# Optimization experiments

Measured on AMD Instinct MI355X. Metric: run time of the kernel, lower is better.

## Reference

```python
import jax, jax.numpy as jnp
import numpy as np

EPS = 1e-6
BASE_TAU = 1.0  # temperature, learnable_tau=False


def setup_inputs() -> dict:
    key = jax.random.key(0)
    k1, k2, k3 = jax.random.split(key, 3)
    n, b, t, h = 16, 4, 2048, 1024
    num_blocks = 24
    return {
        "values": jax.random.normal(k1, (n, b, t, h), dtype=jnp.float32),
        "w_query": jax.random.normal(k2, (num_blocks, h), dtype=jnp.float32) * 0.02,
        "key_pos_bias": jax.random.normal(k3, (num_blocks, h), dtype=jnp.float32) * 0.02,
        "position": 16,
    }


def reference(values, w_query, key_pos_bias, position):
    # values: [n, b, t, h] stacked completed block outputs, n == position
    fp = values.astype(jnp.float32)
    # weight-free RMSNorm (BlockAttnRes._rms_norm)
    inv = jax.lax.rsqrt(jnp.mean(fp * fp, axis=-1, keepdims=True) + EPS)
    keys = fp * inv
    # positional bias for the first `position` block slots
    keys = keys + key_pos_bias[:position].astype(keys.dtype)[:, None, None, :]
    query = w_query[position].astype(jnp.float32)  # [h]
    scale = jnp.sqrt(jnp.float32(values.shape[-1])) * BASE_TAU
    scores = jnp.einsum('h,nbth->nbt', query, keys) / scale  # [n, b, t]
    alpha = jax.nn.softmax(scores, axis=0)                    # softmax over history n
    routed = jnp.einsum('nbt,nbth->bth', alpha, fp).astype(values.dtype)
    alpha_bth = jnp.transpose(alpha, (1, 2, 0))               # [b, t, n]
    return routed, alpha_bth
```

## Files before the change

### kernel.cpp

```cpp
#include <hip/hip_runtime.h>
#include <math.h>

#define H     1024
#define NBLK  16
#define BT    8192
#define ROUTED_SIZE (BT * H)
#define SCALE_INV (1.0f / 32.0f)

__global__ __launch_bounds__(256, 4) void block_attn_res_kernel(
    const float* __restrict__ values,
    const float* __restrict__ w_query,
    const float* __restrict__ key_pos_bias,
    const int*   __restrict__ position_p,
    float*       __restrict__ out)
{
    const int bt   = blockIdx.x;
    const int tid  = threadIdx.x;
    const int lane = tid & 63;
    const int wave = tid >> 6;
    const int h0   = tid << 2;

    const int pos = *position_p;

    const float4 q = *(const float4*)(w_query + (size_t)pos * H + h0);

    float4 v[NBLK];
    const float* vbase = values + (size_t)bt * H + h0;
#pragma unroll
    for (int n = 0; n < NBLK; ++n)
        v[n] = *(const float4*)(vbase + (size_t)n * (size_t)BT * H);

    __shared__ float red[3][NBLK][4];

#pragma unroll
    for (int n = 0; n < NBLK; ++n) {
        const float4 bn = *(const float4*)(key_pos_bias + (size_t)n * H + h0);
        float ss = v[n].x * v[n].x + v[n].y * v[n].y + v[n].z * v[n].z + v[n].w * v[n].w;
        float qv = q.x * v[n].x + q.y * v[n].y + q.z * v[n].z + q.w * v[n].w;
        float qb = q.x * bn.x + q.y * bn.y + q.z * bn.z + q.w * bn.w;
#pragma unroll
        for (int off = 32; off > 0; off >>= 1) {
            ss += __shfl_down(ss, off, 64);
            qv += __shfl_down(qv, off, 64);
            qb += __shfl_down(qb, off, 64);
        }
        if (lane == 0) {
            red[0][n][wave] = ss;
            red[1][n][wave] = qv;
            red[2][n][wave] = qb;
        }
    }
    __syncthreads();

    float score[NBLK];
    float m = -3.402823466e38f;
#pragma unroll
    for (int n = 0; n < NBLK; ++n) {
        const float SS = red[0][n][0] + red[0][n][1] + red[0][n][2] + red[0][n][3];
        const float QV = red[1][n][0] + red[1][n][1] + red[1][n][2] + red[1][n][3];
        const float QB = red[2][n][0] + red[2][n][1] + red[2][n][2] + red[2][n][3];
        const float inv = rsqrtf(SS * (1.0f / (float)H) + 1e-6f);
        score[n] = (inv * QV + QB) * SCALE_INV;
        m = fmaxf(m, score[n]);
    }
    float sum = 0.0f;
#pragma unroll
    for (int n = 0; n < NBLK; ++n) {
        score[n] = __expf(score[n] - m);
        sum += score[n];
    }
    const float rs = 1.0f / sum;

    float4 acc = make_float4(0.0f, 0.0f, 0.0f, 0.0f);
#pragma unroll
    for (int n = 0; n < NBLK; ++n) {
        const float a = score[n] * rs;
        acc.x += a * v[n].x;
        acc.y += a * v[n].y;
        acc.z += a * v[n].z;
        acc.w += a * v[n].w;
    }
    *(float4*)(out + (size_t)bt * H + h0) = acc;

    if (tid < NBLK)
        out[(size_t)ROUTED_SIZE + (size_t)bt * NBLK + tid] = score[tid] * rs;
}

extern "C" void kernel_launch(void* const* d_in, const int* in_sizes, int n_in,
                              void* d_out, int out_size, void* d_ws, size_t ws_size,
                              hipStream_t stream) {
    const float* values       = (const float*)d_in[0];
    const float* w_query      = (const float*)d_in[1];
    const float* key_pos_bias = (const float*)d_in[2];
    const int*   position     = (const int*)d_in[3];
    float*       out          = (float*)d_out;

    hipLaunchKernelGGL(block_attn_res_kernel, dim3(BT), dim3(256), 0, stream,
                       values, w_query, key_pos_bias, position, out);
}
```

Baseline: 715.9 us.

## Precompute query-bias dot products in a separate kernel and halve block size

The query·bias dot products, which are the same for every (b,t), now come from a tiny one-block kernel that writes 16 scalars to workspace. The main kernel no longer reloads the bias rows or does their reduction. The main kernel now uses 128 threads, each holding two float4 slices per history slot, which cuts shuffle work and shared-memory traffic. The cost is a second launch and twice the register pressure per thread (32 float4 values), which could limit occupancy for this memory-bound kernel.

```diff
diff --git a/kernel.cpp b/kernel.cpp
--- a/kernel.cpp
+++ b/kernel.cpp
@@ -7,11 +7,37 @@
 #define ROUTED_SIZE (BT * H)
 #define SCALE_INV (1.0f / 32.0f)
 
-__global__ __launch_bounds__(256, 4) void block_attn_res_kernel(
+__global__ __launch_bounds__(1024) void qb_kernel(
+    const float* __restrict__ w_query,
+    const float* __restrict__ key_pos_bias,
+    const int*   __restrict__ pos_p,
+    float*       __restrict__ qb)
+{
+    const int n    = threadIdx.x >> 6;
+    const int lane = threadIdx.x & 63;
+    const int pos  = *pos_p;
+
+    const float* q = w_query      + (size_t)pos * H;
+    const float* b = key_pos_bias + (size_t)n   * H;
+
+    float s = 0.0f;
+#pragma unroll
+    for (int j = 0; j < 4; ++j) {
+        const int h = lane * 16 + j * 4;
+        const float4 qv = *(const float4*)(q + h);
+        const float4 bv = *(const float4*)(b + h);
+        s += qv.x * bv.x + qv.y * bv.y + qv.z * bv.z + qv.w * bv.w;
+    }
+#pragma unroll
+    for (int off = 32; off; off >>= 1) s += __shfl_xor(s, off, 64);
+    if (lane == 0) qb[n] = s;
+}
+
+__global__ __launch_bounds__(128, 2) void block_attn_res_kernel(
     const float* __restrict__ values,
     const float* __restrict__ w_query,
-    const float* __restrict__ key_pos_bias,
-    const int*   __restrict__ position_p,
+    const int*   __restrict__ pos_p,
+    const float* __restrict__ qb,
     float*       __restrict__ out)
 {
     const int bt   = blockIdx.x;
@@ -19,36 +45,39 @@
     const int lane = tid & 63;
     const int wave = tid >> 6;
     const int h0   = tid << 2;
+    const int h1   = h0 + 512;
 
-    const int pos = *position_p;
+    const int pos = *pos_p;
+    const float4 q0 = *(const float4*)(w_query + (size_t)pos * H + h0);
+    const float4 q1 = *(const float4*)(w_query + (size_t)pos * H + h1);
 
-    const float4 q = *(const float4*)(w_query + (size_t)pos * H + h0);
+    float4 va[NBLK], vb[NBLK];
+    const float* vbase = values + (size_t)bt * H;
+#pragma unroll
+    for (int n = 0; n < NBLK; ++n) {
+        const float* p = vbase + (size_t)n * (size_t)BT * H;
+        va[n] = *(const float4*)(p + h0);
+        vb[n] = *(const float4*)(p + h1);
+    }
 
-    float4 v[NBLK];
-    const float* vbase = values + (size_t)bt * H + h0;
-#pragma unroll
-    for (int n = 0; n < NBLK; ++n)
-        v[n] = *(const float4*)(vbase + (size_t)n * (size_t)BT * H);
-
-    __shared__ float red[3][NBLK][4];
+    __shared__ float red[2][NBLK][2];
 
 #pragma unroll
     for (int n = 0; n < NBLK; ++n) {
-        const float4 bn = *(const float4*)(key_pos_bias + (size_t)n * H + h0);
-        float ss = v[n].x * v[n].x + v[n].y * v[n].y + v[n].z * v[n].z + v[n].w * v[n].w;
-        float qv = q.x * v[n].x + q.y * v[n].y + q.z * v[n].z + q.w * v[n].w;
-        float qb = q.x * bn.x + q.y * bn.y + q.z * bn.z + q.w * bn.w;
+        float ss = va[n].x * va[n].x + va[n].y * va[n].y
+                 + va[n].z * va[n].z + va[n].w * va[n].w
+                 + vb[n].x * vb[n].x + vb[n].y * vb[n].y
+                 + vb[n].z * vb[n].z + vb[n].w * vb[n].w;
+        float qv = q0.x * va[n].x + q0.y * va[n].y
+                 + q0.z * va[n].z + q0.w * va[n].w
+                 + q1.x * vb[n].x + q1.y * vb[n].y
+                 + q1.z * vb[n].z + q1.w * vb[n].w;
 #pragma unroll
-        for (int off = 32; off > 0; off >>= 1) {
-            ss += __shfl_down(ss, off, 64);
-            qv += __shfl_down(qv, off, 64);
-            qb += __shfl_down(qb, off, 64);
+        for (int off = 32; off; off >>= 1) {
+            ss += __shfl_xor(ss, off, 64);
+            qv += __shfl_xor(qv, off, 64);
         }
-        if (lane == 0) {
-            red[0][n][wave] = ss;
-            red[1][n][wave] = qv;
-            red[2][n][wave] = qb;
-        }
+        if (lane == 0) { red[0][n][wave] = ss; red[1][n][wave] = qv; }
     }
     __syncthreads();
 
@@ -56,11 +85,10 @@
     float m = -3.402823466e38f;
 #pragma unroll
     for (int n = 0; n < NBLK; ++n) {
-        const float SS = red[0][n][0] + red[0][n][1] + red[0][n][2] + red[0][n][3];
-        const float QV = red[1][n][0] + red[1][n][1] + red[1][n][2] + red[1][n][3];
-        const float QB = red[2][n][0] + red[2][n][1] + red[2][n][2] + red[2][n][3];
+        const float SS = red[0][n][0] + red[0][n][1];
+        const float QV = red[1][n][0] + red[1][n][1];
         const float inv = rsqrtf(SS * (1.0f / (float)H) + 1e-6f);
-        score[n] = (inv * QV + QB) * SCALE_INV;
+        score[n] = (inv * QV + qb[n]) * SCALE_INV;
         m = fmaxf(m, score[n]);
     }
     float sum = 0.0f;
@@ -71,16 +99,18 @@
     }
     const float rs = 1.0f / sum;
 
-    float4 acc = make_float4(0.0f, 0.0f, 0.0f, 0.0f);
+    float4 acc0 = make_float4(0.f, 0.f, 0.f, 0.f);
+    float4 acc1 = make_float4(0.f, 0.f, 0.f, 0.f);
 #pragma unroll
     for (int n = 0; n < NBLK; ++n) {
         const float a = score[n] * rs;
-        acc.x += a * v[n].x;
-        acc.y += a * v[n].y;
-        acc.z += a * v[n].z;
-        acc.w += a * v[n].w;
+        acc0.x += a * va[n].x;  acc0.y += a * va[n].y;
+        acc0.z += a * va[n].z;  acc0.w += a * va[n].w;
+        acc1.x += a * vb[n].x;  acc1.y += a * vb[n].y;
+        acc1.z += a * vb[n].z;  acc1.w += a * vb[n].w;
     }
-    *(float4*)(out + (size_t)bt * H + h0) = acc;
+    *(float4*)(out + (size_t)bt * H + h0) = acc0;
+    *(float4*)(out + (size_t)bt * H + h1) = acc1;
 
     if (tid < NBLK)
         out[(size_t)ROUTED_SIZE + (size_t)bt * NBLK + tid] = score[tid] * rs;
@@ -94,7 +124,10 @@
     const float* key_pos_bias = (const float*)d_in[2];
     const int*   position     = (const int*)d_in[3];
     float*       out          = (float*)d_out;
+    float*       qb           = (float*)d_ws;
 
-    hipLaunchKernelGGL(block_attn_res_kernel, dim3(BT), dim3(256), 0, stream,
-                       values, w_query, key_pos_bias, position, out);
+    hipLaunchKernelGGL(qb_kernel, dim3(1), dim3(1024), 0, stream,
+                       w_query, key_pos_bias, position, qb);
+    hipLaunchKernelGGL(block_attn_res_kernel, dim3(BT), dim3(128), 0, stream,
+                       values, w_query, position, qb, out);
 }
```

Result: no change. 706.5 us (-1.3%).
